# Kernel optimization log

Hardware: AMD Instinct MI355X
Metric: run time of the kernel (lower is better)

The kernel has to match this reference:

```python
import jax, jax.numpy as jnp
import numpy as np

RANK = 64          # rank
ENT_COMPS = 5      # ent_comps (1 time + 4 space components per rank slot)
REL_COMPS = 4      # rel_comps (quaternion / boost velocity)
N_ENT = 80000
N_REL = 500
B = 2000
INIT_SIZE = 0.001
SCALE = 1.0 / np.sqrt(RANK)
EPS = 1e-9


def _quat_mul(q, p):
    # Hamilton product of quaternions q, p: [..., 4] each, layout (w, x, y, z)
    qw, qx, qy, qz = q[..., 0], q[..., 1], q[..., 2], q[..., 3]
    pw, px, py, pz = p[..., 0], p[..., 1], p[..., 2], p[..., 3]
    return jnp.stack([
        qw * pw - qx * px - qy * py - qz * pz,
        qw * px + qx * pw + qy * pz - qz * py,
        qw * py - qx * pz + qy * pw + qz * px,
        qw * pz + qx * py - qy * px + qz * pw,
    ], axis=-1)


def lorentz_rotate(x, r):
    # x: [B, R, 5] Lorentz vectors (t, s4); r: [B, R, 4] rotation quaternion.
    # Spatial 4D isoclinic rotation via unit-quaternion left multiplication; time fixed.
    q = r * jax.lax.rsqrt(jnp.sum(r * r, axis=-1, keepdims=True) + EPS)
    t, s = x[..., :1], x[..., 1:]
    return jnp.concatenate([t, _quat_mul(q, s)], axis=-1)


def lorentz_boost(x, v):
    # x: [B, R, 5]; v: [B, R, 4] boost velocity (|v| < 1).
    t, s = x[..., :1], x[..., 1:]
    vn2 = jnp.clip(jnp.sum(v * v, axis=-1, keepdims=True), 0.0, 0.999)  # [B,R,1]
    gamma = jax.lax.rsqrt(1.0 - vn2)
    vs = jnp.sum(v * s, axis=-1, keepdims=True)
    t2 = gamma * (t + vs)
    s2 = s + (gamma * t + (gamma - 1.0) * vs / (vn2 + EPS)) * v
    return jnp.concatenate([t2, s2], axis=-1)


def setup_inputs() -> dict:
    key = jax.random.key(0)
    k = jax.random.split(key, 6)
    queries = jax.random.randint(k[0], (B, 3), 0, N_REL, dtype=jnp.int32)
    stru_entities = jax.random.normal(k[1], (N_ENT, 2 * RANK, ENT_COMPS), jnp.float32) * INIT_SIZE
    stru_rel_rotate = jax.random.normal(k[2], (N_REL, RANK, REL_COMPS), jnp.float32) * INIT_SIZE
    stru_rel_boosts = jax.random.normal(k[3], (N_REL, RANK, REL_COMPS), jnp.float32) * INIT_SIZE
    stru_atten = jax.random.normal(k[4], (N_REL, 1, ENT_COMPS * RANK), jnp.float32) * INIT_SIZE
    stru_rel_aux = jax.random.normal(k[5], (N_REL, 2, ENT_COMPS * RANK), jnp.float32) * INIT_SIZE
    return {
        "queries": queries,
        "stru_entities": stru_entities,
        "stru_rel_rotate": stru_rel_rotate,
        "stru_rel_boosts": stru_rel_boosts,
        "stru_atten": stru_atten,
        "stru_rel_aux": stru_rel_aux,
    }


def reference(queries, stru_entities, stru_rel_rotate, stru_rel_boosts, stru_atten, stru_rel_aux):
    b = queries.shape[0]
    D = ENT_COMPS * RANK  # 320
    h, r, t = queries[:, 0], queries[:, 1], queries[:, 2]

    slhs = stru_entities[h]                       # [B, 2R, 5]
    srhs = stru_entities[t]                       # [B, 2R, 5]
    lhs_re = slhs[:, :RANK]                       # [B, R, 5]
    lhs_im = slhs[:, RANK:].reshape(b, D)         # [B, D]
    rhs_re = srhs[:, :RANK].reshape(b, D)
    rhs_im = srhs[:, RANK:].reshape(b, D)

    rrot = stru_rel_rotate[r]                     # [B, R, 4]
    rboost = stru_rel_boosts[r]                   # [B, R, 4]
    atten = stru_atten[r]                         # [B, 1, D]
    aux = stru_rel_aux[r]                         # [B, 2, D]
    aux0, aux1 = aux[:, 0], aux[:, 1]

    to_re = stru_entities[:, :RANK].reshape(N_ENT, D)
    to_im = stru_entities[:, RANK:].reshape(N_ENT, D)

    rot = lorentz_rotate(lhs_re, rrot).reshape(b, D, 1)
    boo = lorentz_boost(lhs_re, rboost).reshape(b, D, 1)
    cands = jnp.concatenate([rot, boo], axis=-1)              # [B, D, 2]
    weights = jax.nn.softmax(jnp.matmul(atten * SCALE, cands), axis=-1)  # [B, 1, 2]
    lhs = jnp.sum(cands * weights, axis=-1)                   # [B, D]

    scores = (lhs * aux0 - lhs_im * aux1) @ to_re.T \
           + (lhs * aux1 + lhs_im * aux0) @ to_im.T           # [B, N_ENT]

    reg0 = jnp.sqrt(lhs_re.reshape(b, D) ** 2 + lhs_im ** 2)
    reg1 = jnp.sqrt(aux0 ** 2 + aux1 ** 2)
    reg2 = jnp.sqrt(rhs_re ** 2 + rhs_im ** 2) * (1.0 / 3.0)
    reg3 = jnp.sqrt(jnp.sum(rrot ** 2, axis=-1))
    reg4 = jnp.sqrt(jnp.sum(rboost ** 2, axis=-1))
    return scores, reg0, reg1, reg2, reg3, reg4
```

## Files before the change

kernel.cpp:

```cpp
#include <hip/hip_runtime.h>
#include <math.h>

#define RANK 64
#define D_DIM 320
#define K_DIM 640
#define N_ENT 80000
#define B_Q 2000
#define M_PAD 2048
#define NT32 20
#define SCALE_F 0.125f
#define EPS_F 1e-9f

#define OFF_SCORES 0ull
#define OFF_REG0 160000000ull
#define OFF_REG1 160640000ull
#define OFF_REG2 161280000ull
#define OFF_REG3 161920000ull
#define OFF_REG4 162048000ull

typedef __attribute__((ext_vector_type(8))) short short8v;
typedef __attribute__((ext_vector_type(4))) float floatx4;

typedef __attribute__((address_space(1))) const unsigned int gu32;
typedef __attribute__((address_space(3))) unsigned int lu32;

#define VMCNT3() asm volatile("s_waitcnt vmcnt(3)" ::: "memory")
#define VMCNT0() asm volatile("s_waitcnt vmcnt(0)" ::: "memory")
#define LGKM0()  asm volatile("s_waitcnt lgkmcnt(0)" ::: "memory")

static __device__ __forceinline__ unsigned short f2bf(float f) {
    union { float f; unsigned int u; } a; a.f = f;
    unsigned int u = a.u;
    u += 0x7FFFu + ((u >> 16) & 1u);
    return (unsigned short)(u >> 16);
}

static __device__ __forceinline__ void prep_row(
    int b, int lane,
    const int* __restrict__ q,
    const float* __restrict__ ent,
    const float* __restrict__ rrot_t,
    const float* __restrict__ rboost_t,
    const float* __restrict__ atten_t,
    const float* __restrict__ aux_t,
    unsigned short* __restrict__ X,
    float* __restrict__ out)
{
    unsigned short* Xrow = X + (size_t)b * K_DIM;

    if (b >= B_Q) {
        #pragma unroll
        for (int c = 0; c < 10; c++) Xrow[lane * 10 + c] = 0;
        return;
    }

    int h = q[3 * b + 0];
    int r = q[3 * b + 1];
    int t = q[3 * b + 2];

    const float* eh = ent + (size_t)h * K_DIM;
    const float* et = ent + (size_t)t * K_DIM;

    float4 rv = *(const float4*)(rrot_t + (size_t)r * 256 + lane * 4);
    float4 bv = *(const float4*)(rboost_t + (size_t)r * 256 + lane * 4);

    const float* xr = eh + lane * 5;
    float x0 = xr[0], x1 = xr[1], x2 = xr[2], x3 = xr[3], x4 = xr[4];

    float rr2 = rv.x * rv.x + rv.y * rv.y + rv.z * rv.z + rv.w * rv.w;
    float rb2 = bv.x * bv.x + bv.y * bv.y + bv.z * bv.z + bv.w * bv.w;

    float qinv = 1.0f / sqrtf(rr2 + EPS_F);
    float qw = rv.x * qinv, qx = rv.y * qinv, qy = rv.z * qinv, qz = rv.w * qinv;
    float pw = x1, px = x2, py = x3, pz = x4;
    float rot[5];
    rot[0] = x0;
    rot[1] = qw * pw - qx * px - qy * py - qz * pz;
    rot[2] = qw * px + qx * pw + qy * pz - qz * py;
    rot[3] = qw * py - qx * pz + qy * pw + qz * px;
    rot[4] = qw * pz + qx * py - qy * px + qz * pw;

    float vn2 = fminf(fmaxf(rb2, 0.0f), 0.999f);
    float sq = sqrtf(1.0f - vn2);
    float gamma = 1.0f / sq;
    float gm1 = vn2 / (sq * (1.0f + sq));
    float vs = bv.x * x1 + bv.y * x2 + bv.z * x3 + bv.w * x4;
    float boo[5];
    boo[0] = gamma * (x0 + vs);
    float coef = gamma * x0 + gm1 * vs / (vn2 + EPS_F);
    boo[1] = x1 + coef * bv.x;
    boo[2] = x2 + coef * bv.y;
    boo[3] = x3 + coef * bv.z;
    boo[4] = x4 + coef * bv.w;

    const float* at = atten_t + (size_t)r * D_DIM + lane * 5;
    float w0 = at[0] * rot[0] + at[1] * rot[1] + at[2] * rot[2] + at[3] * rot[3] + at[4] * rot[4];
    float w1 = at[0] * boo[0] + at[1] * boo[1] + at[2] * boo[2] + at[3] * boo[3] + at[4] * boo[4];
    #pragma unroll
    for (int off = 32; off; off >>= 1) {
        w0 += __shfl_xor(w0, off);
        w1 += __shfl_xor(w1, off);
    }
    w0 *= SCALE_F;
    w1 *= SCALE_F;
    float mx = fmaxf(w0, w1);
    float e0 = expf(w0 - mx), e1 = expf(w1 - mx);
    float inv = 1.0f / (e0 + e1);
    float wt0 = e0 * inv, wt1 = e1 * inv;

    const float* a0p = aux_t + (size_t)r * 640 + lane * 5;
    const float* a1p = a0p + D_DIM;
    float xre[5] = {x0, x1, x2, x3, x4};

    #pragma unroll
    for (int c = 0; c < 5; c++) {
        int d = lane * 5 + c;
        float lhs = wt0 * rot[c] + wt1 * boo[c];
        float im = eh[D_DIM + d];
        float a0 = a0p[c], a1 = a1p[c];
        Xrow[d]         = f2bf(lhs * a0 - im * a1);
        Xrow[D_DIM + d] = f2bf(lhs * a1 + im * a0);
        out[OFF_REG0 + (size_t)b * D_DIM + d] = sqrtf(xre[c] * xre[c] + im * im);
        out[OFF_REG1 + (size_t)b * D_DIM + d] = sqrtf(a0 * a0 + a1 * a1);
        float tre = et[d], tim = et[D_DIM + d];
        out[OFF_REG2 + (size_t)b * D_DIM + d] = sqrtf(tre * tre + tim * tim) * (1.0f / 3.0f);
    }
    out[OFF_REG3 + (size_t)b * RANK + lane] = sqrtf(rr2);
    out[OFF_REG4 + (size_t)b * RANK + lane] = sqrtf(rb2);
}

#define PREP_BLKS 512
#define CONV_BLKS 2048
__global__ __launch_bounds__(256) void prepconv_kernel(
    const int* __restrict__ q,
    const float* __restrict__ ent,
    const float* __restrict__ rrot_t,
    const float* __restrict__ rboost_t,
    const float* __restrict__ atten_t,
    const float* __restrict__ aux_t,
    unsigned short* __restrict__ X,
    unsigned short* __restrict__ Eb,
    float* __restrict__ out)
{
    if (blockIdx.x < PREP_BLKS) {
        int b = blockIdx.x * 4 + (threadIdx.x >> 6);
        prep_row(b, threadIdx.x & 63, q, ent, rrot_t, rboost_t, atten_t, aux_t, X, out);
    } else {
        const size_t n4 = (size_t)N_ENT * K_DIM / 4;
        size_t stride = (size_t)CONV_BLKS * 256;
        for (size_t v = (size_t)(blockIdx.x - PREP_BLKS) * 256 + threadIdx.x; v < n4; v += stride) {
            float4 f = ((const float4*)ent)[v];
            ushort4 u;
            u.x = f2bf(f.x); u.y = f2bf(f.y); u.z = f2bf(f.z); u.w = f2bf(f.w);
            ((ushort4*)Eb)[v] = u;
        }
    }
}

__global__ __launch_bounds__(64) void prep_kernel(
    const int* __restrict__ q, const float* __restrict__ ent,
    const float* __restrict__ rrot_t, const float* __restrict__ rboost_t,
    const float* __restrict__ atten_t, const float* __restrict__ aux_t,
    unsigned short* __restrict__ X, float* __restrict__ out)
{
    prep_row(blockIdx.x, threadIdx.x, q, ent, rrot_t, rboost_t, atten_t, aux_t, X, out);
}

__global__ __launch_bounds__(512, 4) void gemm256b(
    const unsigned short* __restrict__ X,
    const unsigned short* __restrict__ Eb,
    float* __restrict__ C)
{
    __shared__ unsigned short lds[36864];

    const int tid = threadIdx.x;
    const int lane = tid & 63;
    const int wid = tid >> 6;
    const int wm = wid >> 1;
    const int wn = wid & 1;

    const int bid = blockIdx.x;
    const int m0 = (bid & 7) * 256;
    const int n0 = (bid >> 3) * 128;

    const int fr = lane & 15;
    const int kq = lane >> 4;
    const int cbs8 = (kq ^ ((fr >> 1) & 3)) * 8;

    floatx4 acc[4][4];
    #pragma unroll
    for (int i = 0; i < 4; i++)
        #pragma unroll
        for (int j = 0; j < 4; j++) acc[i][j] = (floatx4)0.0f;

    int aoff[4], boff[4];
    #pragma unroll
    for (int i = 0; i < 4; i++) aoff[i] = (wm * 64 + i * 16 + fr) * 32 + cbs8;
    #pragma unroll
    for (int j = 0; j < 4; j++) boff[j] = 8192 + (wn * 64 + j * 16 + fr) * 32 + cbs8;

    const int srow = tid >> 2;
    const int sslot = tid & 3;
    const int scolg = (sslot ^ ((srow >> 1) & 3)) * 8;
    const unsigned short* gA0 = X + (size_t)(m0 + srow) * K_DIM + scolg;
    const unsigned short* gA1 = X + (size_t)(m0 + 128 + srow) * K_DIM + scolg;
    const unsigned short* gB  = Eb + (size_t)(n0 + srow) * K_DIM + scolg;
    const int ldst = tid * 8;

    auto stage = [&](int bufS , int kt) {
        const int base = bufS * 12288;
        __builtin_amdgcn_global_load_lds((gu32*)(gA0 + kt * 32), (lu32*)&lds[base + ldst],        16, 0, 0);
        __builtin_amdgcn_global_load_lds((gu32*)(gA1 + kt * 32), (lu32*)&lds[base + 4096 + ldst], 16, 0, 0);
        __builtin_amdgcn_global_load_lds((gu32*)(gB  + kt * 32), (lu32*)&lds[base + 8192 + ldst], 16, 0, 0);
    };

#define PHASE_BODY(BASE, STAGE_STMT, WAITM)                                   \
    {                                                                         \
        short8v a_[4], b_[4];                                                 \
        _Pragma("unroll")                                                     \
        for (int i = 0; i < 4; i++) a_[i] = *(const short8v*)&lds[(BASE) + aoff[i]]; \
        _Pragma("unroll")                                                     \
        for (int j = 0; j < 4; j++) b_[j] = *(const short8v*)&lds[(BASE) + boff[j]]; \
        STAGE_STMT;                                                           \
        WAITM();                                                              \
        __builtin_amdgcn_s_barrier();                                         \
        LGKM0();                                                              \
        __builtin_amdgcn_sched_barrier(0);                                    \
        __builtin_amdgcn_s_setprio(1);                                        \
        _Pragma("unroll")                                                     \
        for (int i = 0; i < 4; i++)                                           \
            _Pragma("unroll")                                                 \
            for (int j = 0; j < 4; j++)                                       \
                acc[i][j] = __builtin_amdgcn_mfma_f32_16x16x32_bf16(          \
                    a_[i], b_[j], acc[i][j], 0, 0, 0);                        \
        __builtin_amdgcn_s_setprio(0);                                        \
        __builtin_amdgcn_s_barrier();                                         \
    }

    stage(0, 0);
    stage(1, 1);
    VMCNT0();
    __builtin_amdgcn_s_barrier();

    int bR = 0;
    for (int t = 0; t < NT32 - 2; ++t) {
        int bS = bR + 2; if (bS >= 3) bS -= 3;
        PHASE_BODY(bR * 12288, stage(bS, t + 2), VMCNT3)
        bR = (bR + 1 == 3) ? 0 : bR + 1;
    }
    PHASE_BODY(0, (void)0, VMCNT0)
    PHASE_BODY(12288, (void)0, VMCNT0)
#undef PHASE_BODY

    const int rb = kq * 4;
    #pragma unroll
    for (int i = 0; i < 4; i++) {
        #pragma unroll
        for (int j = 0; j < 4; j++) {
            int row = m0 + wm * 64 + i * 16 + rb;
            int col = n0 + wn * 64 + j * 16 + fr;
            #pragma unroll
            for (int r = 0; r < 4; r++) {
                if (row + r < B_Q)
                    C[(size_t)(row + r) * N_ENT + col] = acc[i][j][r];
            }
        }
    }
}

__global__ __launch_bounds__(256) void gemm_mfma_fb(
    const unsigned short* __restrict__ X,
    const float* __restrict__ Ef,
    float* __restrict__ C)
{
    __shared__ unsigned short As[128 * 32];
    __shared__ unsigned short Bs[128 * 32];

    const int tid = threadIdx.x;
    const int lane = tid & 63;
    const int wave = tid >> 6;
    const int wm = wave >> 1, wn = wave & 1;
    const int m0 = blockIdx.x * 128;
    const int n0 = blockIdx.y * 128;

    floatx4 acc[4][4];
    #pragma unroll
    for (int i = 0; i < 4; i++)
        #pragma unroll
        for (int j = 0; j < 4; j++) acc[i][j] = (floatx4)0.0f;

    const int srow = tid >> 2;
    const int scol = (tid & 3) * 8;
    const int fr = lane & 15;
    const int kb = (lane >> 4) * 8;
    const int brow_f = tid >> 1;
    const int bcol_f = (tid & 1) * 16;

    for (int k0 = 0; k0 < K_DIM; k0 += 32) {
        __syncthreads();
        #pragma unroll
        for (int r = 0; r < 2; r++) {
            const unsigned short* gp = X + (size_t)(m0 + srow + r * 64) * K_DIM + k0 + scol;
            __builtin_amdgcn_global_load_lds((gu32*)gp, (lu32*)(As + (size_t)(r * 64 + srow) * 32 + scol), 16, 0, 0);
        }
        {
            const float* ep = Ef + (size_t)(n0 + brow_f) * K_DIM + k0 + bcol_f;
            float4 f0 = *(const float4*)(ep);
            float4 f1 = *(const float4*)(ep + 4);
            float4 f2 = *(const float4*)(ep + 8);
            float4 f3 = *(const float4*)(ep + 12);
            short8v p0, p1;
            p0[0] = (short)f2bf(f0.x); p0[1] = (short)f2bf(f0.y);
            p0[2] = (short)f2bf(f0.z); p0[3] = (short)f2bf(f0.w);
            p0[4] = (short)f2bf(f1.x); p0[5] = (short)f2bf(f1.y);
            p0[6] = (short)f2bf(f1.z); p0[7] = (short)f2bf(f1.w);
            p1[0] = (short)f2bf(f2.x); p1[1] = (short)f2bf(f2.y);
            p1[2] = (short)f2bf(f2.z); p1[3] = (short)f2bf(f2.w);
            p1[4] = (short)f2bf(f3.x); p1[5] = (short)f2bf(f3.y);
            p1[6] = (short)f2bf(f3.z); p1[7] = (short)f2bf(f3.w);
            *(short8v*)(Bs + (size_t)brow_f * 32 + bcol_f) = p0;
            *(short8v*)(Bs + (size_t)brow_f * 32 + bcol_f + 8) = p1;
        }
        __syncthreads();

        short8v a[4], b[4];
        #pragma unroll
        for (int i = 0; i < 4; i++)
            a[i] = *(const short8v*)(As + (size_t)(wm * 64 + i * 16 + fr) * 32 + kb);
        #pragma unroll
        for (int j = 0; j < 4; j++)
            b[j] = *(const short8v*)(Bs + (size_t)(wn * 64 + j * 16 + fr) * 32 + kb);

        #pragma unroll
        for (int i = 0; i < 4; i++)
            #pragma unroll
            for (int j = 0; j < 4; j++)
                acc[i][j] = __builtin_amdgcn_mfma_f32_16x16x32_bf16(a[i], b[j], acc[i][j], 0, 0, 0);
    }

    const int rbase = (lane >> 4) * 4;
    #pragma unroll
    for (int i = 0; i < 4; i++) {
        #pragma unroll
        for (int j = 0; j < 4; j++) {
            int row = m0 + wm * 64 + i * 16 + rbase;
            int col = n0 + wn * 64 + j * 16 + fr;
            #pragma unroll
            for (int r = 0; r < 4; r++) {
                if (row + r < B_Q)
                    C[(size_t)(row + r) * N_ENT + col] = acc[i][j][r];
            }
        }
    }
}

extern "C" void kernel_launch(void* const* d_in, const int* in_sizes, int n_in,
                              void* d_out, int out_size, void* d_ws, size_t ws_size,
                              hipStream_t stream) {
    const int* queries = (const int*)d_in[0];
    const float* ent = (const float*)d_in[1];
    const float* rrot = (const float*)d_in[2];
    const float* rboost = (const float*)d_in[3];
    const float* atten = (const float*)d_in[4];
    const float* aux = (const float*)d_in[5];
    float* out = (float*)d_out;

    unsigned short* X = (unsigned short*)d_ws;
    const size_t offE = (size_t)M_PAD * K_DIM * 2;
    const size_t needE = (size_t)N_ENT * K_DIM * 2;
    unsigned short* Eb = (unsigned short*)((char*)d_ws + offE);
    bool pre = (ws_size >= offE + needE);

    if (pre) {
        prepconv_kernel<<<PREP_BLKS + CONV_BLKS, 256, 0, stream>>>(
            queries, ent, rrot, rboost, atten, aux, X, Eb, out);
        gemm256b<<<8 * 625, 512, 0, stream>>>(X, Eb, out + OFF_SCORES);
    } else {
        prep_kernel<<<M_PAD, 64, 0, stream>>>(queries, ent, rrot, rboost, atten, aux, X, out);
        dim3 grid(M_PAD / 128, N_ENT / 128);
        gemm_mfma_fb<<<grid, 256, 0, stream>>>(X, ent, out + OFF_SCORES);
    }
}
```

Baseline: 448.4 us.

## Enlarge GEMM tile to 1024x128 with double-buffered LDS and 8x8 MFMA per wave

Replaces the 256x128 block tile with a 1024x128 tile where each of 8 waves computes a 128x128 sub-tile using an 8x8 grid of MFMA accumulators. The goal is to cut redundant loads of the entity matrix, which is now read only twice instead of eight times, and to raise the MFMA-to-LDS-read ratio. The pipeline goes from triple buffering with a partial vmcnt wait to double buffering with a full wait each iteration, and occupancy drops to one block per CU. The 256 accumulator registers per thread and the 1250-block grid risk register spills, exposed load latency and poor CU balance.

```diff
diff --git a/kernel.cpp b/kernel.cpp
--- a/kernel.cpp
+++ b/kernel.cpp
@@ -24,7 +24,6 @@
 typedef __attribute__((address_space(1))) const unsigned int gu32;
 typedef __attribute__((address_space(3))) unsigned int lu32;
 
-#define VMCNT3() asm volatile("s_waitcnt vmcnt(3)" ::: "memory")
 #define VMCNT0() asm volatile("s_waitcnt vmcnt(0)" ::: "memory")
 #define LGKM0()  asm volatile("s_waitcnt lgkmcnt(0)" ::: "memory")
 
@@ -166,99 +165,91 @@
     prep_row(blockIdx.x, threadIdx.x, q, ent, rrot_t, rboost_t, atten_t, aux_t, X, out);
 }
 
-__global__ __launch_bounds__(512, 4) void gemm256b(
+#define BUFO2 36864
+
+__global__ __launch_bounds__(512, 1) void gemm1024(
     const unsigned short* __restrict__ X,
     const unsigned short* __restrict__ Eb,
     float* __restrict__ C)
 {
-    __shared__ unsigned short lds[36864];
+    __shared__ unsigned short lds[73728];
 
     const int tid = threadIdx.x;
     const int lane = tid & 63;
     const int wid = tid >> 6;
-    const int wm = wid >> 1;
-    const int wn = wid & 1;
 
     const int bid = blockIdx.x;
-    const int m0 = (bid & 7) * 256;
-    const int n0 = (bid >> 3) * 128;
+    const int m0 = (bid & 1) * 1024;
+    const int n0 = (bid >> 1) * 128;
 
     const int fr = lane & 15;
     const int kq = lane >> 4;
     const int cbs8 = (kq ^ ((fr >> 1) & 3)) * 8;
 
-    floatx4 acc[4][4];
-    #pragma unroll
-    for (int i = 0; i < 4; i++)
-        #pragma unroll
-        for (int j = 0; j < 4; j++) acc[i][j] = (floatx4)0.0f;
-
-    int aoff[4], boff[4];
-    #pragma unroll
-    for (int i = 0; i < 4; i++) aoff[i] = (wm * 64 + i * 16 + fr) * 32 + cbs8;
-    #pragma unroll
-    for (int j = 0; j < 4; j++) boff[j] = 8192 + (wn * 64 + j * 16 + fr) * 32 + cbs8;
+    floatx4 acc[8][8];
+    #pragma unroll
+    for (int i = 0; i < 8; i++)
+        #pragma unroll
+        for (int j = 0; j < 8; j++) acc[i][j] = (floatx4)0.0f;
+
+    int aoff[8], boff[8];
+    #pragma unroll
+    for (int i = 0; i < 8; i++) aoff[i] = (wid * 128 + i * 16 + fr) * 32 + cbs8;
+    #pragma unroll
+    for (int j = 0; j < 8; j++) boff[j] = 32768 + (j * 16 + fr) * 32 + cbs8;
 
     const int srow = tid >> 2;
-    const int sslot = tid & 3;
-    const int scolg = (sslot ^ ((srow >> 1) & 3)) * 8;
-    const unsigned short* gA0 = X + (size_t)(m0 + srow) * K_DIM + scolg;
-    const unsigned short* gA1 = X + (size_t)(m0 + 128 + srow) * K_DIM + scolg;
-    const unsigned short* gB  = Eb + (size_t)(n0 + srow) * K_DIM + scolg;
-    const int ldst = tid * 8;
-
-    auto stage = [&](int bufS , int kt) {
-        const int base = bufS * 12288;
-        __builtin_amdgcn_global_load_lds((gu32*)(gA0 + kt * 32), (lu32*)&lds[base + ldst],        16, 0, 0);
-        __builtin_amdgcn_global_load_lds((gu32*)(gA1 + kt * 32), (lu32*)&lds[base + 4096 + ldst], 16, 0, 0);
-        __builtin_amdgcn_global_load_lds((gu32*)(gB  + kt * 32), (lu32*)&lds[base + 8192 + ldst], 16, 0, 0);
+    const int scolg = ((tid & 3) ^ ((srow >> 1) & 3)) * 8;
+
+    auto stage = [&](int bufOff, int kt) {
+        #pragma unroll
+        for (int l = 0; l < 8; l++) {
+            const unsigned short* gp = X + (size_t)(m0 + l * 128 + srow) * K_DIM + kt * 32 + scolg;
+            __builtin_amdgcn_global_load_lds((gu32*)gp,
+                (lu32*)&lds[bufOff + l * 4096 + tid * 8], 16, 0, 0);
+        }
+        const unsigned short* gb = Eb + (size_t)(n0 + srow) * K_DIM + kt * 32 + scolg;
+        __builtin_amdgcn_global_load_lds((gu32*)gb,
+            (lu32*)&lds[bufOff + 32768 + tid * 8], 16, 0, 0);
     };
 
-#define PHASE_BODY(BASE, STAGE_STMT, WAITM)                                   \
-    {                                                                         \
-        short8v a_[4], b_[4];                                                 \
-        _Pragma("unroll")                                                     \
-        for (int i = 0; i < 4; i++) a_[i] = *(const short8v*)&lds[(BASE) + aoff[i]]; \
-        _Pragma("unroll")                                                     \
-        for (int j = 0; j < 4; j++) b_[j] = *(const short8v*)&lds[(BASE) + boff[j]]; \
-        STAGE_STMT;                                                           \
-        WAITM();                                                              \
-        __builtin_amdgcn_s_barrier();                                         \
-        LGKM0();                                                              \
-        __builtin_amdgcn_sched_barrier(0);                                    \
-        __builtin_amdgcn_s_setprio(1);                                        \
-        _Pragma("unroll")                                                     \
-        for (int i = 0; i < 4; i++)                                           \
-            _Pragma("unroll")                                                 \
-            for (int j = 0; j < 4; j++)                                       \
-                acc[i][j] = __builtin_amdgcn_mfma_f32_16x16x32_bf16(          \
-                    a_[i], b_[j], acc[i][j], 0, 0, 0);                        \
-        __builtin_amdgcn_s_setprio(0);                                        \
-        __builtin_amdgcn_s_barrier();                                         \
-    }
-
     stage(0, 0);
-    stage(1, 1);
     VMCNT0();
     __builtin_amdgcn_s_barrier();
 
-    int bR = 0;
-    for (int t = 0; t < NT32 - 2; ++t) {
-        int bS = bR + 2; if (bS >= 3) bS -= 3;
-        PHASE_BODY(bR * 12288, stage(bS, t + 2), VMCNT3)
-        bR = (bR + 1 == 3) ? 0 : bR + 1;
-    }
-    PHASE_BODY(0, (void)0, VMCNT0)
-    PHASE_BODY(12288, (void)0, VMCNT0)
-#undef PHASE_BODY
+    int bufo = 0;
+    for (int t = 0; t < NT32; t++) {
+        short8v a_[8], b_[8];
+        #pragma unroll
+        for (int i = 0; i < 8; i++) a_[i] = *(const short8v*)&lds[bufo + aoff[i]];
+        #pragma unroll
+        for (int j = 0; j < 8; j++) b_[j] = *(const short8v*)&lds[bufo + boff[j]];
+
+        if (t < NT32 - 1) stage(bufo ^ BUFO2, t + 1);
+
+        LGKM0();
+        __builtin_amdgcn_sched_barrier(0);
+        __builtin_amdgcn_s_setprio(1);
+        #pragma unroll
+        for (int i = 0; i < 8; i++)
+            #pragma unroll
+            for (int j = 0; j < 8; j++)
+                acc[i][j] = __builtin_amdgcn_mfma_f32_16x16x32_bf16(
+                    a_[i], b_[j], acc[i][j], 0, 0, 0);
+        __builtin_amdgcn_s_setprio(0);
+
+        VMCNT0();
+        __builtin_amdgcn_s_barrier();
+        bufo ^= BUFO2;
+    }
 
     const int rb = kq * 4;
     #pragma unroll
-    for (int i = 0; i < 4; i++) {
-        #pragma unroll
-        for (int j = 0; j < 4; j++) {
-            int row = m0 + wm * 64 + i * 16 + rb;
-            int col = n0 + wn * 64 + j * 16 + fr;
+    for (int i = 0; i < 8; i++) {
+        int row = m0 + wid * 128 + i * 16 + rb;
+        #pragma unroll
+        for (int j = 0; j < 8; j++) {
+            int col = n0 + j * 16 + fr;
             #pragma unroll
             for (int r = 0; r < 4; r++) {
                 if (row + r < B_Q)
@@ -374,7 +365,7 @@
     if (pre) {
         prepconv_kernel<<<PREP_BLKS + CONV_BLKS, 256, 0, stream>>>(
             queries, ent, rrot, rboost, atten, aux, X, Eb, out);
-        gemm256b<<<8 * 625, 512, 0, stream>>>(X, Eb, out + OFF_SCORES);
+        gemm1024<<<2 * 625, 512, 0, stream>>>(X, Eb, out + OFF_SCORES);
     } else {
         prep_kernel<<<M_PAD, 64, 0, stream>>>(queries, ent, rrot, rboost, atten, aux, X, out);
         dim3 grid(M_PAD / 128, N_ENT / 128);
```

New measurement: 1.751 ms. +290.5%, slower.

## Enlarge GEMM tile to 256x256 with four-stage LDS pipeline and nontemporal stores

Applied to the files above, without the earlier changes.

The scores GEMM tile grows from 256x128 to 256x256 per 512-thread block. Each wave now computes a 128x64 sub-tile, which halves the number of blocks and raises arithmetic intensity per LDS byte. The LDS ring deepens from three to four buffers with three loads in flight, and one of the two per-step barriers is dropped. Output is written with nontemporal stores, and N edge rows are clamped because 80000 is not a multiple of 256. In exchange, the 32 accumulator tiles per wave raise register pressure and lower occupancy, and the final partial N tile wastes work.

```diff
diff --git a/kernel.cpp b/kernel.cpp
--- a/kernel.cpp
+++ b/kernel.cpp
@@ -7,6 +7,7 @@
 #define N_ENT 80000
 #define B_Q 2000
 #define M_PAD 2048
+#define NBLK_N 313
 #define NT32 20
 #define SCALE_F 0.125f
 #define EPS_F 1e-9f
@@ -24,7 +25,8 @@
 typedef __attribute__((address_space(1))) const unsigned int gu32;
 typedef __attribute__((address_space(3))) unsigned int lu32;
 
-#define VMCNT3() asm volatile("s_waitcnt vmcnt(3)" ::: "memory")
+#define VMCNT8() asm volatile("s_waitcnt vmcnt(8)" ::: "memory")
+#define VMCNT4() asm volatile("s_waitcnt vmcnt(4)" ::: "memory")
 #define VMCNT0() asm volatile("s_waitcnt vmcnt(0)" ::: "memory")
 #define LGKM0()  asm volatile("s_waitcnt lgkmcnt(0)" ::: "memory")
 
@@ -166,69 +168,75 @@
     prep_row(blockIdx.x, threadIdx.x, q, ent, rrot_t, rboost_t, atten_t, aux_t, X, out);
 }
 
-__global__ __launch_bounds__(512, 4) void gemm256b(
+#define BUFSZ 16384
+
+__global__ __launch_bounds__(512) void gemm256c(
     const unsigned short* __restrict__ X,
     const unsigned short* __restrict__ Eb,
     float* __restrict__ C)
 {
-    __shared__ unsigned short lds[36864];
+    __shared__ unsigned short lds[4 * BUFSZ];
 
     const int tid = threadIdx.x;
     const int lane = tid & 63;
     const int wid = tid >> 6;
-    const int wm = wid >> 1;
-    const int wn = wid & 1;
+    const int wm = wid >> 2;
+    const int wn = wid & 3;
 
     const int bid = blockIdx.x;
     const int m0 = (bid & 7) * 256;
-    const int n0 = (bid >> 3) * 128;
+    const int n0 = (bid >> 3) * 256;
 
     const int fr = lane & 15;
     const int kq = lane >> 4;
     const int cbs8 = (kq ^ ((fr >> 1) & 3)) * 8;
 
-    floatx4 acc[4][4];
-    #pragma unroll
-    for (int i = 0; i < 4; i++)
+    floatx4 acc[8][4];
+    #pragma unroll
+    for (int i = 0; i < 8; i++)
         #pragma unroll
         for (int j = 0; j < 4; j++) acc[i][j] = (floatx4)0.0f;
 
-    int aoff[4], boff[4];
-    #pragma unroll
-    for (int i = 0; i < 4; i++) aoff[i] = (wm * 64 + i * 16 + fr) * 32 + cbs8;
+    int aoff[8], boff[4];
+    #pragma unroll
+    for (int i = 0; i < 8; i++) aoff[i] = (wm * 128 + i * 16 + fr) * 32 + cbs8;
     #pragma unroll
     for (int j = 0; j < 4; j++) boff[j] = 8192 + (wn * 64 + j * 16 + fr) * 32 + cbs8;
 
     const int srow = tid >> 2;
-    const int sslot = tid & 3;
-    const int scolg = (sslot ^ ((srow >> 1) & 3)) * 8;
-    const unsigned short* gA0 = X + (size_t)(m0 + srow) * K_DIM + scolg;
-    const unsigned short* gA1 = X + (size_t)(m0 + 128 + srow) * K_DIM + scolg;
-    const unsigned short* gB  = Eb + (size_t)(n0 + srow) * K_DIM + scolg;
-    const int ldst = tid * 8;
-
-    auto stage = [&](int bufS , int kt) {
-        const int base = bufS * 12288;
-        __builtin_amdgcn_global_load_lds((gu32*)(gA0 + kt * 32), (lu32*)&lds[base + ldst],        16, 0, 0);
-        __builtin_amdgcn_global_load_lds((gu32*)(gA1 + kt * 32), (lu32*)&lds[base + 4096 + ldst], 16, 0, 0);
-        __builtin_amdgcn_global_load_lds((gu32*)(gB  + kt * 32), (lu32*)&lds[base + 8192 + ldst], 16, 0, 0);
+    const int scolg = ((tid & 3) ^ ((srow >> 1) & 3)) * 8;
+
+    auto stage = [&](int bufBase , int kt) {
+        #pragma unroll
+        for (int l = 0; l < 2; l++) {
+            const unsigned short* ga = X + (size_t)(m0 + l * 128 + srow) * K_DIM + kt * 32 + scolg;
+            __builtin_amdgcn_global_load_lds((gu32*)ga,
+                (lu32*)&lds[bufBase + l * 4096 + tid * 8], 16, 0, 0);
+        }
+        #pragma unroll
+        for (int l = 0; l < 2; l++) {
+            int grow = n0 + l * 128 + srow;
+            if (grow > N_ENT - 1) grow = N_ENT - 1;
+            const unsigned short* gb = Eb + (size_t)grow * K_DIM + kt * 32 + scolg;
+            __builtin_amdgcn_global_load_lds((gu32*)gb,
+                (lu32*)&lds[bufBase + 8192 + l * 4096 + tid * 8], 16, 0, 0);
+        }
     };
 
-#define PHASE_BODY(BASE, STAGE_STMT, WAITM)                                   \
+#define KSTEP(BUFB, STAGE_STMT, WAIT_STMT)                                    \
     {                                                                         \
-        short8v a_[4], b_[4];                                                 \
+        short8v a_[8], b_[4];                                                 \
         _Pragma("unroll")                                                     \
-        for (int i = 0; i < 4; i++) a_[i] = *(const short8v*)&lds[(BASE) + aoff[i]]; \
+        for (int i = 0; i < 8; i++) a_[i] = *(const short8v*)&lds[(BUFB) + aoff[i]]; \
         _Pragma("unroll")                                                     \
-        for (int j = 0; j < 4; j++) b_[j] = *(const short8v*)&lds[(BASE) + boff[j]]; \
+        for (int j = 0; j < 4; j++) b_[j] = *(const short8v*)&lds[(BUFB) + boff[j]]; \
         STAGE_STMT;                                                           \
-        WAITM();                                                              \
-        __builtin_amdgcn_s_barrier();                                         \
+        WAIT_STMT;                                                            \
         LGKM0();                                                              \
         __builtin_amdgcn_sched_barrier(0);                                    \
         __builtin_amdgcn_s_setprio(1);                                        \
         _Pragma("unroll")                                                     \
-        for (int i = 0; i < 4; i++)                                           \
+        for (int i = 0; i < 8; i++)                                           \
             _Pragma("unroll")                                                 \
             for (int j = 0; j < 4; j++)                                       \
                 acc[i][j] = __builtin_amdgcn_mfma_f32_16x16x32_bf16(          \
@@ -237,32 +245,36 @@
         __builtin_amdgcn_s_barrier();                                         \
     }
 
-    stage(0, 0);
-    stage(1, 1);
+    stage(0 * BUFSZ, 0);
+    stage(1 * BUFSZ, 1);
+    stage(2 * BUFSZ, 2);
     VMCNT0();
     __builtin_amdgcn_s_barrier();
 
-    int bR = 0;
-    for (int t = 0; t < NT32 - 2; ++t) {
-        int bS = bR + 2; if (bS >= 3) bS -= 3;
-        PHASE_BODY(bR * 12288, stage(bS, t + 2), VMCNT3)
-        bR = (bR + 1 == 3) ? 0 : bR + 1;
-    }
-    PHASE_BODY(0, (void)0, VMCNT0)
-    PHASE_BODY(12288, (void)0, VMCNT0)
-#undef PHASE_BODY
+    for (int t = 0; t < NT32 - 3; t++) {
+        const int bufb = (t & 3) * BUFSZ;
+        const int stgb = ((t + 3) & 3) * BUFSZ;
+        KSTEP(bufb, stage(stgb, t + 3), VMCNT8())
+    }
+    KSTEP((17 & 3) * BUFSZ, (void)0, VMCNT4())
+    KSTEP((18 & 3) * BUFSZ, (void)0, VMCNT0())
+    KSTEP((19 & 3) * BUFSZ, (void)0, (void)0)
+#undef KSTEP
 
     const int rb = kq * 4;
     #pragma unroll
-    for (int i = 0; i < 4; i++) {
+    for (int i = 0; i < 8; i++) {
+        int row = m0 + wm * 128 + i * 16 + rb;
         #pragma unroll
         for (int j = 0; j < 4; j++) {
-            int row = m0 + wm * 64 + i * 16 + rb;
             int col = n0 + wn * 64 + j * 16 + fr;
-            #pragma unroll
-            for (int r = 0; r < 4; r++) {
-                if (row + r < B_Q)
-                    C[(size_t)(row + r) * N_ENT + col] = acc[i][j][r];
+            if (col < N_ENT) {
+                #pragma unroll
+                for (int r = 0; r < 4; r++) {
+                    if (row + r < B_Q)
+                        __builtin_nontemporal_store(acc[i][j][r],
+                            &C[(size_t)(row + r) * N_ENT + col]);
+                }
             }
         }
     }
@@ -374,7 +386,7 @@
     if (pre) {
         prepconv_kernel<<<PREP_BLKS + CONV_BLKS, 256, 0, stream>>>(
             queries, ent, rrot, rboost, atten, aux, X, Eb, out);
-        gemm256b<<<8 * 625, 512, 0, stream>>>(X, Eb, out + OFF_SCORES);
+        gemm256c<<<8 * NBLK_N, 512, 0, stream>>>(X, Eb, out + OFF_SCORES);
     } else {
         prep_kernel<<<M_PAD, 64, 0, stream>>>(queries, ent, rrot, rboost, atten, aux, X, out);
         dim3 grid(M_PAD / 128, N_ENT / 128);
```

Measured after the change: 390.7 us. 12.9% less time.
